# Kernel tuning notes

Measured on AMD Instinct MI355X. Metric: run time of the kernel, lower is better.

The kernel has to match this reference:

```python
import jax, jax.numpy as jnp
import numpy as np

D_MODEL = 4096
N_TYPES = 6  # fixed event_types list in the module


def setup_inputs() -> dict:
    key = jax.random.key(0)
    ks = jax.random.split(key, 7)
    E, B, d = 131072, 16384, D_MODEL
    return {
        "event_type": jax.random.randint(ks[0], (E,), 0, N_TYPES),
        "confidence": jax.random.uniform(ks[1], (E,), jnp.float32),
        "location": jax.random.uniform(ks[2], (E, 2), jnp.float32) * jnp.array([640.0, 480.0], jnp.float32),
        "batch_idx": jax.random.randint(ks[3], (E,), 0, B),
        "batch_size": B,
        "type_emb": jax.random.normal(ks[4], (N_TYPES, d // 4), jnp.float32),
        "W1": jax.random.normal(ks[5], (d // 2, d // 4 + 3), jnp.float32) / np.sqrt(d // 4 + 3).astype(np.float32),
        "b1": jnp.zeros((d // 2,), jnp.float32),
        "W2": jax.random.normal(ks[6], (d, d // 2), jnp.float32) / np.sqrt(d // 2).astype(np.float32),
        "b2": jnp.zeros((d,), jnp.float32),
    }


def reference(event_type, confidence, location, batch_idx, batch_size, type_emb, W1, b1, W2, b2):
    E = confidence.shape[0]
    B = batch_size
    # per-batch-slot max confidence (empty slots -> -inf)
    seg_max = jax.ops.segment_max(confidence, batch_idx, num_segments=B)
    is_top = confidence == seg_max[batch_idx]
    # first event attaining the max (matches torch's max-over-list semantics)
    cand = jnp.where(is_top, jnp.arange(E), E)
    top_idx = jnp.full((B,), E, dtype=cand.dtype).at[batch_idx].min(cand)
    has_event = top_idx < E
    safe_idx = jnp.where(has_event, top_idx, 0)

    emb = type_emb[event_type[safe_idx]]                 # [B, d/4]
    c = confidence[safe_idx][:, None]                    # [B, 1]
    loc = location[safe_idx] / jnp.array([640.0, 480.0], jnp.float32)  # [B, 2]
    feats = jnp.concatenate([emb, c, loc], axis=-1)      # [B, d/4 + 3]

    h = jax.nn.relu(feats @ W1.T + b1)                   # [B, d/2]
    out = h @ W2.T + b2                                  # [B, d]
    return jnp.where(has_event[:, None], out, jnp.zeros((), out.dtype))
```

## Files before the change

### kernel.cpp

```cpp
#include <hip/hip_runtime.h>
#include <hip/hip_bf16.h>

#define NT 6
#define BM 256
#define BN 256
#define BK 32
#define SLOT 16384

typedef __attribute__((ext_vector_type(4))) float f32x4;
typedef __attribute__((ext_vector_type(16))) float f32x16;
typedef __attribute__((ext_vector_type(8))) short bf16x8;

__device__ __forceinline__ short f2bf(float f) {
    __hip_bfloat16 h = __float2bfloat16(f);
    return (short)__builtin_bit_cast(unsigned short, h);
}

__global__ void k_segmax(const float* __restrict__ conf,
                         const int* __restrict__ bidx,
                         unsigned long long* __restrict__ packed, int E) {
    int i = blockIdx.x * blockDim.x + threadIdx.x;
    if (i >= E) return;
    unsigned cb = __float_as_uint(conf[i]);
    unsigned long long p = ((unsigned long long)cb << 32) | (unsigned)(~(unsigned)i);
    atomicMax(&packed[bidx[i]], p);
}

__global__ void k_base(const float* __restrict__ emb, const float* __restrict__ W1,
                       const float* __restrict__ b1, float* __restrict__ base,
                       float* __restrict__ vecs, int d2, int d4) {
    int gw = (blockIdx.x * blockDim.x + threadIdx.x) >> 6;
    int lane = threadIdx.x & 63;
    int t = gw / d2, n = gw % d2;
    const float* e = emb + (size_t)t * d4;
    const float* w = W1 + (size_t)n * (d4 + 3);
    float s = 0.f;
    for (int k = lane; k < d4; k += 64) s += e[k] * w[k];
#pragma unroll
    for (int m = 32; m; m >>= 1) s += __shfl_xor(s, m);
    if (lane == 0) {
        base[gw] = s + b1[n];
        if (t == 0) {
            vecs[n]          = w[d4];
            vecs[d2 + n]     = w[d4 + 1];
            vecs[2 * d2 + n] = w[d4 + 2];
        }
    }
}

__global__ void k_w2cast(const float* __restrict__ W2, short* __restrict__ W2b, long n) {
    long i = ((long)blockIdx.x * blockDim.x + threadIdx.x) * 8;
    if (i >= n) return;
    bf16x8 v;
#pragma unroll
    for (int j = 0; j < 8; ++j) v[j] = f2bf(W2[i + j]);
    *(bf16x8*)(W2b + i) = v;
}

__global__ void k_h(const unsigned long long* __restrict__ packed,
                    const int* __restrict__ etype, const float* __restrict__ loc,
                    const float* __restrict__ base, const float* __restrict__ vecs,
                    float* __restrict__ mask, short* __restrict__ h, int d2) {
    int b = blockIdx.x;
    int tid = threadIdx.x;
    unsigned long long p = packed[b];
    bool has = (p != 0ULL);
    float conf = 0.f, lx = 0.f, ly = 0.f;
    int t = 0;
    if (has) {
        unsigned idx = ~(unsigned)(p & 0xFFFFFFFFu);
        conf = __uint_as_float((unsigned)(p >> 32));
        t  = etype[idx];
        lx = loc[2 * (size_t)idx]     * (1.0f / 640.0f);
        ly = loc[2 * (size_t)idx + 1] * (1.0f / 480.0f);
    }
    if (tid == 0) mask[b] = has ? 1.0f : 0.0f;
    const float* bs = base + (size_t)t * d2;
    const float* cv = vecs;
    const float* xv = vecs + d2;
    const float* yv = vecs + 2 * d2;
    int n0 = tid * 8;
    bf16x8 v;
#pragma unroll
    for (int j = 0; j < 8; ++j) {
        int n = n0 + j;
        float g = bs[n] + conf * cv[n] + lx * xv[n] + ly * yv[n];
        g = fmaxf(g, 0.f);
        v[j] = has ? f2bf(g) : (short)0;
    }
    *(bf16x8*)(h + (size_t)b * d2 + n0) = v;
}


#define GLL(src, dst) __builtin_amdgcn_global_load_lds(                      \
    (const __attribute__((address_space(1))) void*)(src),                    \
    (__attribute__((address_space(3))) void*)(dst), 16, 0, 0)

#define STAGE4(slotp) do {                                                   \
    GLL(pa0, (slotp) + dA0); GLL(pa1, (slotp) + dA1);                        \
    GLL(pb0, (slotp) + dB0); GLL(pb1, (slotp) + dB1);                        \
    pa0 += BK; pa1 += BK; pb0 += BK; pb1 += BK; } while (0)

__global__ __launch_bounds__(512, 2)
void k_gemm(const short* __restrict__ A, const short* __restrict__ Bm,
            const float* __restrict__ b2, const float* __restrict__ mask,
            float* __restrict__ C, int M, int N, int K, int nbn) {
    __shared__ __align__(16) short lds[4 * SLOT];

    int tid = threadIdx.x;
    int lane = tid & 63;
    int wave = tid >> 6;
    int wr = wave >> 2, wc = wave & 3;

    int bid = blockIdx.x;
    int wg = (bid & 7) * ((int)gridDim.x >> 3) + (bid >> 3);
    int bm = wg / nbn, bn = wg % nbn;
    int row0 = bm * BM, col0 = bn * BN;

    int srow = tid >> 2;
    int chunkL = (tid & 3) ^ ((srow >> 1) & 3);
    const short* pa0 = A + (size_t)(row0 + srow) * K + chunkL * 8;
    const short* pa1 = pa0 + (size_t)128 * K;
    const short* pb0 = Bm + (size_t)(col0 + srow) * K + chunkL * 8;
    const short* pb1 = pb0 + (size_t)128 * K;
    int dA0 = tid * 8, dA1 = 4096 + tid * 8;
    int dB0 = 8192 + tid * 8, dB1 = 12288 + tid * 8;

    int l31 = lane & 31, kh = lane >> 5;
    int g = (l31 >> 1) & 3;
    int cp0 = kh ^ g;
    int cp1 = (2 + kh) ^ g;
    int aoff = (wr * 128 + l31) * 32;
    int boff = 8192 + (wc * 64 + l31) * 32;

    f32x16 acc[4][2] = {};
    bf16x8 af[4][2], bf_[2][2];

    int KT = K / BK;

    STAGE4(lds + 0 * SLOT);
    STAGE4(lds + 1 * SLOT);
    STAGE4(lds + 2 * SLOT);
    asm volatile("s_waitcnt vmcnt(8)" ::: "memory");
    __builtin_amdgcn_s_barrier();

#pragma unroll 1
    for (int t = 0; t < KT; ++t) {
        const short* sr = lds + (t & 3) * SLOT;
        bf_[0][0] = *(const bf16x8*)(sr + boff + cp0 * 8);
        bf_[0][1] = *(const bf16x8*)(sr + boff + cp1 * 8);
        bf_[1][0] = *(const bf16x8*)(sr + boff + 1024 + cp0 * 8);
        bf_[1][1] = *(const bf16x8*)(sr + boff + 1024 + cp1 * 8);
        af[0][0] = *(const bf16x8*)(sr + aoff + cp0 * 8);
        af[0][1] = *(const bf16x8*)(sr + aoff + cp1 * 8);
        af[1][0] = *(const bf16x8*)(sr + aoff + 1024 + cp0 * 8);
        af[1][1] = *(const bf16x8*)(sr + aoff + 1024 + cp1 * 8);
        if (t < KT - 3) {
            short* sw = lds + ((t + 3) & 3) * SLOT;
            STAGE4(sw);
        }
        af[2][0] = *(const bf16x8*)(sr + aoff + 2048 + cp0 * 8);
        af[2][1] = *(const bf16x8*)(sr + aoff + 2048 + cp1 * 8);
        af[3][0] = *(const bf16x8*)(sr + aoff + 3072 + cp0 * 8);
        af[3][1] = *(const bf16x8*)(sr + aoff + 3072 + cp1 * 8);

        __builtin_amdgcn_s_setprio(1);
#pragma unroll
        for (int m = 0; m < 4; ++m)
#pragma unroll
            for (int n2 = 0; n2 < 2; ++n2) {
                acc[m][n2] = __builtin_amdgcn_mfma_f32_32x32x16_bf16(
                    af[m][0], bf_[n2][0], acc[m][n2], 0, 0, 0);
                acc[m][n2] = __builtin_amdgcn_mfma_f32_32x32x16_bf16(
                    af[m][1], bf_[n2][1], acc[m][n2], 0, 0, 0);
            }
        __builtin_amdgcn_s_setprio(0);

        if (t < KT - 1) {
            if (t < KT - 3)       asm volatile("s_waitcnt vmcnt(8)" ::: "memory");
            else if (t == KT - 3) asm volatile("s_waitcnt vmcnt(4)" ::: "memory");
            else                  asm volatile("s_waitcnt vmcnt(0)" ::: "memory");
            __builtin_amdgcn_s_barrier();
        }
    }

#pragma unroll
    for (int m = 0; m < 4; ++m) {
        int rb = row0 + wr * 128 + m * 32 + 4 * kh;
#pragma unroll
        for (int q = 0; q < 4; ++q) {
#pragma unroll
            for (int j = 0; j < 4; ++j) {
                int r = rb + 8 * q + j;
                float mk = mask[r];
#pragma unroll
                for (int n2 = 0; n2 < 2; ++n2) {
                    int c = col0 + wc * 64 + n2 * 32 + l31;
                    C[(size_t)r * N + c] = (acc[m][n2][q * 4 + j] + b2[c]) * mk;
                }
            }
        }
    }
}

extern "C" void kernel_launch(void* const* d_in, const int* in_sizes, int n_in,
                              void* d_out, int out_size, void* d_ws, size_t ws_size,
                              hipStream_t stream) {
    const int* etype   = (const int*)d_in[0];
    const float* conf  = (const float*)d_in[1];
    const float* loc   = (const float*)d_in[2];
    const int* bidx    = (const int*)d_in[3];
    const float* emb   = (const float*)d_in[5];
    const float* W1    = (const float*)d_in[6];
    const float* b1    = (const float*)d_in[7];
    const float* W2    = (const float*)d_in[8];
    const float* b2    = (const float*)d_in[9];
    float* out = (float*)d_out;

    int E  = in_sizes[0];
    int d2 = in_sizes[7];
    int d  = in_sizes[9];
    int d4 = in_sizes[5] / NT;
    int B  = out_size / d;

    char* ws = (char*)d_ws;
    unsigned long long* packed = (unsigned long long*)ws;
    float* mask = (float*)(ws + (size_t)B * 8);
    float* base = mask + B;
    float* vecs = base + NT * d2;
    short* w2b  = (short*)(vecs + 3 * d2);
    short* h    = w2b + (size_t)d * d2;

    hipMemsetAsync(packed, 0, (size_t)B * 8, stream);
    k_segmax<<<(E + 255) / 256, 256, 0, stream>>>(conf, bidx, packed, E);
    k_base<<<(NT * d2) / 4, 256, 0, stream>>>(emb, W1, b1, base, vecs, d2, d4);
    long nw2 = (long)d * d2;
    k_w2cast<<<(int)(nw2 / 8 / 256), 256, 0, stream>>>(W2, w2b, nw2);
    k_h<<<B, 256, 0, stream>>>(packed, etype, loc, base, vecs, mask, h, d2);
    int nbm = B / BM, nbn = d / BN;
    k_gemm<<<dim3(nbm * nbn), dim3(512), 0, stream>>>(h, w2b, b2, mask, out, B, d, d2, nbn);
}
```

Before: 350.9 us.

## Switch GEMM inner loop to 16x16x32 MFMA with split LDS waits

Replaces the 32x32x16 bf16 MFMA tiling with 16x16x32 MFMAs over an 8x4 accumulator grid per wave, recomputing the LDS fragment offsets and swizzle to match. The A fragments are split into two halves, and explicit lgkmcnt waits with scheduling barriers let the first 16 MFMAs start while the second half of the LDS reads is still in flight. The epilogue is rewritten for the 16x16 output layout. The intent is better overlap of LDS reads with matrix math; the cost is more MFMA instructions per K step and a more fragile hand-made schedule.

```diff
diff --git a/kernel.cpp b/kernel.cpp
--- a/kernel.cpp
+++ b/kernel.cpp
@@ -8,7 +8,6 @@
 #define SLOT 16384
 
 typedef __attribute__((ext_vector_type(4))) float f32x4;
-typedef __attribute__((ext_vector_type(16))) float f32x16;
 typedef __attribute__((ext_vector_type(8))) short bf16x8;
 
 __device__ __forceinline__ short f2bf(float f) {
@@ -101,6 +100,8 @@
     GLL(pb0, (slotp) + dB0); GLL(pb1, (slotp) + dB1);                        \
     pa0 += BK; pa1 += BK; pb0 += BK; pb1 += BK; } while (0)
 
+#define SB __builtin_amdgcn_sched_barrier(0)
+
 __global__ __launch_bounds__(512, 2)
 void k_gemm(const short* __restrict__ A, const short* __restrict__ Bm,
             const float* __restrict__ b2, const float* __restrict__ mask,
@@ -126,15 +127,12 @@
     int dA0 = tid * 8, dA1 = 4096 + tid * 8;
     int dB0 = 8192 + tid * 8, dB1 = 12288 + tid * 8;
 
-    int l31 = lane & 31, kh = lane >> 5;
-    int g = (l31 >> 1) & 3;
-    int cp0 = kh ^ g;
-    int cp1 = (2 + kh) ^ g;
-    int aoff = (wr * 128 + l31) * 32;
-    int boff = 8192 + (wc * 64 + l31) * 32;
-
-    f32x16 acc[4][2] = {};
-    bf16x8 af[4][2], bf_[2][2];
+    int frow = lane & 15, fk = lane >> 4;
+    int cp = fk ^ ((frow >> 1) & 3);
+    int aoff = (wr * 128 + frow) * 32 + cp * 8;
+    int boff = 8192 + (wc * 64 + frow) * 32 + cp * 8;
+
+    f32x4 acc[8][4] = {};
 
     int KT = K / BK;
 
@@ -147,35 +145,41 @@
 #pragma unroll 1
     for (int t = 0; t < KT; ++t) {
         const short* sr = lds + (t & 3) * SLOT;
-        bf_[0][0] = *(const bf16x8*)(sr + boff + cp0 * 8);
-        bf_[0][1] = *(const bf16x8*)(sr + boff + cp1 * 8);
-        bf_[1][0] = *(const bf16x8*)(sr + boff + 1024 + cp0 * 8);
-        bf_[1][1] = *(const bf16x8*)(sr + boff + 1024 + cp1 * 8);
-        af[0][0] = *(const bf16x8*)(sr + aoff + cp0 * 8);
-        af[0][1] = *(const bf16x8*)(sr + aoff + cp1 * 8);
-        af[1][0] = *(const bf16x8*)(sr + aoff + 1024 + cp0 * 8);
-        af[1][1] = *(const bf16x8*)(sr + aoff + 1024 + cp1 * 8);
+        bf16x8 afA[4], afB[4], bv[4];
+#pragma unroll
+        for (int n = 0; n < 4; ++n)
+            bv[n] = *(const bf16x8*)(sr + boff + n * 512);
+#pragma unroll
+        for (int m = 0; m < 4; ++m)
+            afA[m] = *(const bf16x8*)(sr + aoff + m * 512);
+        SB;
+#pragma unroll
+        for (int m = 0; m < 4; ++m)
+            afB[m] = *(const bf16x8*)(sr + aoff + 2048 + m * 512);
         if (t < KT - 3) {
             short* sw = lds + ((t + 3) & 3) * SLOT;
             STAGE4(sw);
         }
-        af[2][0] = *(const bf16x8*)(sr + aoff + 2048 + cp0 * 8);
-        af[2][1] = *(const bf16x8*)(sr + aoff + 2048 + cp1 * 8);
-        af[3][0] = *(const bf16x8*)(sr + aoff + 3072 + cp0 * 8);
-        af[3][1] = *(const bf16x8*)(sr + aoff + 3072 + cp1 * 8);
-
+        SB;
+        asm volatile("s_waitcnt lgkmcnt(4)" ::: "memory");
+        SB;
         __builtin_amdgcn_s_setprio(1);
 #pragma unroll
         for (int m = 0; m < 4; ++m)
 #pragma unroll
-            for (int n2 = 0; n2 < 2; ++n2) {
-                acc[m][n2] = __builtin_amdgcn_mfma_f32_32x32x16_bf16(
-                    af[m][0], bf_[n2][0], acc[m][n2], 0, 0, 0);
-                acc[m][n2] = __builtin_amdgcn_mfma_f32_32x32x16_bf16(
-                    af[m][1], bf_[n2][1], acc[m][n2], 0, 0, 0);
-            }
+            for (int n = 0; n < 4; ++n)
+                acc[m][n] = __builtin_amdgcn_mfma_f32_16x16x32_bf16(
+                    afA[m], bv[n], acc[m][n], 0, 0, 0);
+        SB;
+        asm volatile("s_waitcnt lgkmcnt(0)" ::: "memory");
+        SB;
+#pragma unroll
+        for (int m = 0; m < 4; ++m)
+#pragma unroll
+            for (int n = 0; n < 4; ++n)
+                acc[4 + m][n] = __builtin_amdgcn_mfma_f32_16x16x32_bf16(
+                    afB[m], bv[n], acc[4 + m][n], 0, 0, 0);
         __builtin_amdgcn_s_setprio(0);
-
         if (t < KT - 1) {
             if (t < KT - 3)       asm volatile("s_waitcnt vmcnt(8)" ::: "memory");
             else if (t == KT - 3) asm volatile("s_waitcnt vmcnt(4)" ::: "memory");
@@ -185,19 +189,16 @@
     }
 
 #pragma unroll
-    for (int m = 0; m < 4; ++m) {
-        int rb = row0 + wr * 128 + m * 32 + 4 * kh;
-#pragma unroll
-        for (int q = 0; q < 4; ++q) {
-#pragma unroll
-            for (int j = 0; j < 4; ++j) {
-                int r = rb + 8 * q + j;
-                float mk = mask[r];
-#pragma unroll
-                for (int n2 = 0; n2 < 2; ++n2) {
-                    int c = col0 + wc * 64 + n2 * 32 + l31;
-                    C[(size_t)r * N + c] = (acc[m][n2][q * 4 + j] + b2[c]) * mk;
-                }
+    for (int m = 0; m < 8; ++m) {
+        int rbase = row0 + wr * 128 + m * 16 + (lane >> 4) * 4;
+#pragma unroll
+        for (int j = 0; j < 4; ++j) {
+            int r = rbase + j;
+            float mk = mask[r];
+#pragma unroll
+            for (int n = 0; n < 4; ++n) {
+                int c = col0 + wc * 64 + n * 16 + frow;
+                C[(size_t)r * N + c] = (acc[m][n][j] + b2[c]) * mk;
             }
         }
     }
```

After: 312.0 us. -11.1%, faster.
